# Kernel tuning notes

Hardware: AMD Instinct MI355X
Metric: run time of the kernel (lower is better)

Reference implementation:

```python
import jax, jax.numpy as jnp
import numpy as np

B, N, D = 4, 2048, 512
H, DH = 8, 64  # heads, dim_head; inner_dim = H*DH = 512
SCALE = DH ** -0.5


def setup_inputs() -> dict:
    key = jax.random.key(0)
    kx, kw = jax.random.split(key)
    x = jax.random.normal(kx, (B, N, D), dtype=jnp.float32)
    # torch Linear weight layout: [out_features=3*H*DH, in_features=D]
    W_qkv = jax.random.normal(kw, (3 * H * DH, D), dtype=jnp.float32) * 0.02
    return {"x": x, "W_qkv": W_qkv}


def reference(x, W_qkv):
    b, n, d = x.shape
    # qkv projection (no bias since qkv_bias=False)
    qkv = x @ W_qkv.T                                  # [b, n, 3*H*DH]
    qkv = qkv.reshape(b, n, 3, H, DH).transpose(2, 0, 3, 1, 4)  # [3, b, H, n, DH]
    q, k, v = qkv[0], qkv[1], qkv[2]
    # shifted query: q_cross[t] = q[t-1] for t>=1, q_cross[0] = q[0]
    q_cross = jnp.concatenate([q[:, :, :1, :], q[:, :, :-1, :]], axis=2)
    scores = jnp.einsum("bhqd,bhkd->bhqk", q_cross * SCALE, k)  # [b, H, n, n]
    attn = jax.nn.softmax(scores, axis=-1)
    out = jnp.einsum("bhqk,bhkd->bhqd", attn, v)       # [b, H, n, DH]
    out = out.transpose(0, 2, 1, 3).reshape(b, n, H * DH)
    # to_out is Dropout(0.0) -> identity in eval / p=0
    return out
```

## Files before the change

### kernel.cpp

```cpp
#include <hip/hip_runtime.h>
#include <hip/hip_bf16.h>
#include <stdint.h>

typedef __bf16 bf16_t;
typedef float floatx4 __attribute__((ext_vector_type(4)));
typedef __bf16 bf16x8 __attribute__((ext_vector_type(8)));
typedef __bf16 bf16x4 __attribute__((ext_vector_type(4)));
typedef unsigned int uintx4 __attribute__((ext_vector_type(4)));

#define QSCALE 0.1803368801111204f

__device__ __forceinline__ void gl2lds16(const bf16_t* g, bf16_t* l) {
    __builtin_amdgcn_global_load_lds(
        (const __attribute__((address_space(1))) unsigned int*)g,
        (__attribute__((address_space(3))) unsigned int*)l,
        16, 0, 0);
}

__device__ __forceinline__ unsigned pk2(float lo, float hi) {
    unsigned short a = __builtin_bit_cast(unsigned short, (bf16_t)lo);
    unsigned short b = __builtin_bit_cast(unsigned short, (bf16_t)hi);
    return (unsigned)a | ((unsigned)b << 16);
}

__global__ __launch_bounds__(256) void convert_kernel(const float* __restrict__ x,
                                                      bf16_t* __restrict__ xb,
                                                      const float* __restrict__ w,
                                                      bf16_t* __restrict__ wb,
                                                      int nx4) {
    int i = blockIdx.x * 256 + threadIdx.x;
    const float* in; bf16_t* out; int j;
    if (i < nx4) { in = x; out = xb; j = i; }
    else         { in = w; out = wb; j = i - nx4; }
    float4 v = ((const float4*)in)[j];
    bf16x4 o;
    o.x = (bf16_t)v.x; o.y = (bf16_t)v.y; o.z = (bf16_t)v.z; o.w = (bf16_t)v.w;
    ((bf16x4*)out)[j] = o;
}

__global__ __launch_bounds__(256) void qkv_gemm(const bf16_t* __restrict__ X,
                                                const bf16_t* __restrict__ W,
                                                bf16_t* __restrict__ Q,
                                                bf16_t* __restrict__ K,
                                                bf16_t* __restrict__ Vt)
{
    __shared__ bf16_t As[128 * 64];
    __shared__ bf16_t Bs[128 * 64];

    const int tid  = threadIdx.x;
    const int wave = tid >> 6;
    const int lane = tid & 63;
    const int quad = lane >> 4;
    const int lrow = lane & 15;
    const int t7g  = lrow & 7;
    const int bm0 = blockIdx.x * 128;
    const int bn0 = blockIdx.y * 128;
    const int mw = (wave >> 1) * 64;
    const int nw = (wave & 1) * 64;
    const int wbase = tid & 192;

    floatx4 acc[4][4];
#pragma unroll
    for (int i = 0; i < 4; i++)
#pragma unroll
        for (int j = 0; j < 4; j++) acc[i][j] = (floatx4)0.0f;

#pragma unroll 1
    for (int kb = 0; kb < 8; ++kb) {
        const int k0 = kb * 64;
        __syncthreads();
#pragma unroll
        for (int r = 0; r < 4; ++r) {
            int c = r * 256 + tid;
            int row = c >> 3, kc = c & 7;
            int skc = kc ^ (row & 7);
            gl2lds16(X + (size_t)(bm0 + row) * 512 + k0 + skc * 8,
                     As + (size_t)(r * 256 + wbase) * 8);
        }
#pragma unroll
        for (int r = 0; r < 4; ++r) {
            int c = r * 256 + tid;
            int row = c >> 3, kc = c & 7;
            int skc = kc ^ (row & 7);
            gl2lds16(W + (size_t)(bn0 + row) * 512 + k0 + skc * 8,
                     Bs + (size_t)(r * 256 + wbase) * 8);
        }
        __syncthreads();
#pragma unroll
        for (int ks = 0; ks < 2; ++ks) {
            bf16x8 af[4], bfr[4];
#pragma unroll
            for (int mi = 0; mi < 4; mi++)
                af[mi] = *(const bf16x8*)(As + (mw + mi * 16 + lrow) * 64 + (((ks * 4 + quad) ^ t7g) << 3));
#pragma unroll
            for (int ni = 0; ni < 4; ni++)
                bfr[ni] = *(const bf16x8*)(Bs + (nw + ni * 16 + lrow) * 64 + (((ks * 4 + quad) ^ t7g) << 3));
#pragma unroll
            for (int mi = 0; mi < 4; mi++)
#pragma unroll
                for (int ni = 0; ni < 4; ni++)
                    acc[mi][ni] = __builtin_amdgcn_mfma_f32_16x16x32_bf16(af[mi], bfr[ni], acc[mi][ni], 0, 0, 0);
        }
    }

#pragma unroll
    for (int mi = 0; mi < 4; mi++) {
        int mbase = bm0 + mw + mi * 16 + quad * 4;
        int b = mbase >> 11, n = mbase & 2047;
#pragma unroll
        for (int ni = 0; ni < 4; ni++) {
            int o = bn0 + nw + ni * 16 + lrow;
            int s  = o >> 9;
            int h  = (o >> 6) & 7;
            int dh = o & 63;
            int bh = b * 8 + h;
            if (s == 2) {
                bf16x4 pv;
#pragma unroll
                for (int r = 0; r < 4; r++) pv[r] = (bf16_t)acc[mi][ni][r];
                *(bf16x4*)(Vt + ((size_t)bh * 64 + dh) * 2048 + n) = pv;
            } else if (s == 0) {
#pragma unroll
                for (int r = 0; r < 4; r++)
                    Q[((size_t)bh * 2048 + n + r) * 64 + dh] = (bf16_t)(acc[mi][ni][r] * QSCALE);
            } else {
#pragma unroll
                for (int r = 0; r < 4; r++)
                    K[((size_t)bh * 2048 + n + r) * 64 + dh] = (bf16_t)acc[mi][ni][r];
            }
        }
    }
}

__device__ __forceinline__ void stage_tile(const bf16_t* __restrict__ kb,
                                           const bf16_t* __restrict__ vb,
                                           int kt, bf16_t* ksbuf, bf16_t* vsbuf,
                                           int wave, int lane) {
#pragma unroll
    for (int part = 0; part < 2; ++part) {
        int ch  = part * 256 + wave * 64 + lane;
        int row = ch >> 3, cc = ch & 7;
        int scc = cc ^ (row & 7);
        bf16_t* ldst = ksbuf + (size_t)(part * 256 + wave * 64) * 8;
        gl2lds16(kb + ((size_t)(kt * 64 + row)) * 64 + scc * 8, ldst);
        bf16_t* ldst2 = vsbuf + (size_t)(part * 256 + wave * 64) * 8;
        gl2lds16(vb + (size_t)row * 2048 + kt * 64 + scc * 8, ldst2);
    }
}

__global__ __launch_bounds__(256, 5) void flash_attn(const bf16_t* __restrict__ Q,
                                                     const bf16_t* __restrict__ K,
                                                     const bf16_t* __restrict__ Vt,
                                                     float* __restrict__ Out)
{
    __shared__ bf16_t Ks[2][64 * 64];
    __shared__ bf16_t Vs[2][64 * 64];

    const int tid  = threadIdx.x;
    const int wave = tid >> 6;
    const int lane = tid & 63;
    const int quad = lane >> 4;
    const int c    = lane & 15;
    const int t7   = c & 7;
    const int qhalf = wave >> 1;
    const int khalf = wave & 1;
    const int qt = blockIdx.x;
    const int bh = blockIdx.y;
    const int b = bh >> 3, h = bh & 7;

    const int bw    = ((c & 4) << 1) | ((c & 8) >> 1) | (c & 3);
    const int brow7 = bw & 7;

    bf16x8 qf[2][2];
#pragma unroll
    for (int mt = 0; mt < 2; ++mt) {
        int qg  = qt * 64 + qhalf * 32 + mt * 16 + c;
        int src = (qg == 0) ? 0 : qg - 1;
        const bf16_t* qbase = Q + ((size_t)bh * 2048 + src) * 64;
        qf[mt][0] = *(const bf16x8*)(qbase + quad * 8);
        qf[mt][1] = *(const bf16x8*)(qbase + 32 + quad * 8);
    }

    floatx4 o[2][4];
#pragma unroll
    for (int mt = 0; mt < 2; ++mt)
#pragma unroll
        for (int i = 0; i < 4; i++) o[mt][i] = (floatx4)0.0f;
    float lacc[2] = {0.f, 0.f};

    const bf16_t* kb = K + ((size_t)bh * 2048) * 64;
    const bf16_t* vb = Vt + ((size_t)bh * 64) * 2048;

    stage_tile(kb, vb, 0, Ks[0], Vs[0], wave, lane);

#pragma unroll 1
    for (int kt = 0; kt < 32; ++kt) {
        const int buf = kt & 1;
        __syncthreads();
        if (kt < 31)
            stage_tile(kb, vb, kt + 1, Ks[buf ^ 1], Vs[buf ^ 1], wave, lane);

        const bf16_t* ks = Ks[buf];
        const bf16_t* vs = Vs[buf];

        floatx4 s[2][2];
        __builtin_amdgcn_s_setprio(1);
#pragma unroll
        for (int nt = 0; nt < 2; ++nt) {
            const bf16_t* krow = ks + (khalf * 32 + nt * 16 + bw) * 64;
            bf16x8 kf0 = *(const bf16x8*)(krow + ((quad ^ brow7) << 3));
            bf16x8 kf1 = *(const bf16x8*)(krow + (((4 + quad) ^ brow7) << 3));
#pragma unroll
            for (int mt = 0; mt < 2; ++mt) {
                floatx4 t = (floatx4)0.0f;
                t = __builtin_amdgcn_mfma_f32_16x16x32_bf16(kf0, qf[mt][0], t, 0, 0, 0);
                t = __builtin_amdgcn_mfma_f32_16x16x32_bf16(kf1, qf[mt][1], t, 0, 0, 0);
                s[mt][nt] = t;
            }
        }
        __builtin_amdgcn_s_setprio(0);

        bf16x8 pfrag[2];
#pragma unroll
        for (int mt = 0; mt < 2; ++mt) {
            float pe[2][4];
#pragma unroll
            for (int nt = 0; nt < 2; ++nt)
#pragma unroll
                for (int r = 0; r < 4; ++r) {
                    float p = __builtin_amdgcn_exp2f(s[mt][nt][r]);
                    lacc[mt] += p;
                    pe[nt][r] = p;
                }
            unsigned A0 = pk2(pe[0][0], pe[0][1]);
            unsigned A1 = pk2(pe[0][2], pe[0][3]);
            unsigned B0 = pk2(pe[1][0], pe[1][1]);
            unsigned B1 = pk2(pe[1][2], pe[1][3]);
            auto r0 = __builtin_amdgcn_permlane32_swap((int)A0, (int)B0, false, false);
            auto r1 = __builtin_amdgcn_permlane32_swap((int)A1, (int)B1, false, false);
            uintx4 fd;
            fd.x = (unsigned)r0[0];
            fd.y = (unsigned)r1[0];
            fd.z = (unsigned)r0[1];
            fd.w = (unsigned)r1[1];
            pfrag[mt] = __builtin_bit_cast(bf16x8, fd);
        }

        __builtin_amdgcn_s_setprio(1);
#pragma unroll
        for (int sub = 0; sub < 4; ++sub) {
            const bf16_t* vrow = vs + (sub * 16 + c) * 64;
            bf16x8 vf = *(const bf16x8*)(vrow + (((khalf * 4 + quad) ^ t7) << 3));
            o[0][sub] = __builtin_amdgcn_mfma_f32_16x16x32_bf16(pfrag[0], vf, o[0][sub], 0, 0, 0);
            o[1][sub] = __builtin_amdgcn_mfma_f32_16x16x32_bf16(pfrag[1], vf, o[1][sub], 0, 0, 0);
        }
        __builtin_amdgcn_s_setprio(0);
    }

#pragma unroll
    for (int mt = 0; mt < 2; ++mt) {
        lacc[mt] += __shfl_xor(lacc[mt], 16, 64);
        lacc[mt] += __shfl_xor(lacc[mt], 32, 64);
    }

    __syncthreads();
    float* obuf = (float*)Ks;
    float* lbuf = (float*)Vs;
    if (khalf == 1) {
#pragma unroll
        for (int mt = 0; mt < 2; ++mt)
#pragma unroll
            for (int sub = 0; sub < 4; ++sub)
                *(floatx4*)(obuf + qhalf * 2048 + (mt * 4 + sub) * 256 + lane * 4) = o[mt][sub];
        if (lane < 16) {
#pragma unroll
            for (int mt = 0; mt < 2; ++mt)
                lbuf[qhalf * 32 + mt * 16 + c] = lacc[mt];
        }
    }
    __syncthreads();
    if (khalf == 0) {
#pragma unroll
        for (int mt = 0; mt < 2; ++mt)
#pragma unroll
            for (int sub = 0; sub < 4; ++sub)
                o[mt][sub] += *(const floatx4*)(obuf + qhalf * 2048 + (mt * 4 + sub) * 256 + lane * 4);
#pragma unroll
        for (int mt = 0; mt < 2; ++mt)
            lacc[mt] += lbuf[qhalf * 32 + mt * 16 + c];

        float* ob = Out + (size_t)b * 2048 * 512 + (size_t)h * 64;
#pragma unroll
        for (int mt = 0; mt < 2; ++mt) {
            int n0 = qt * 64 + qhalf * 32 + mt * 16 + quad * 4;
#pragma unroll
            for (int r = 0; r < 4; r++) {
                float lr = __shfl(lacc[mt], quad * 4 + r, 64);
                float inv = 1.0f / lr;
                float* orow = ob + (size_t)(n0 + r) * 512;
#pragma unroll
                for (int sub = 0; sub < 4; ++sub)
                    orow[sub * 16 + c] = o[mt][sub][r] * inv;
            }
        }
    }
}

extern "C" void kernel_launch(void* const* d_in, const int* in_sizes, int n_in,
                              void* d_out, int out_size, void* d_ws, size_t ws_size,
                              hipStream_t stream) {
    const float* x = (const float*)d_in[0];
    const float* w = (const float*)d_in[1];
    float* out = (float*)d_out;

    char* ws = (char*)d_ws;
    bf16_t* xb = (bf16_t*)(ws);
    bf16_t* wb = (bf16_t*)(ws + 8388608);
    bf16_t* q  = (bf16_t*)(ws + 9961472);
    bf16_t* k  = (bf16_t*)(ws + 18350080);
    bf16_t* vt = (bf16_t*)(ws + 26738688);

    convert_kernel<<<4864, 256, 0, stream>>>(x, xb, w, wb, 1048576);
    qkv_gemm<<<dim3(64, 12), 256, 0, stream>>>(xb, wb, q, k, vt);
    flash_attn<<<dim3(32, 32), 256, 0, stream>>>(q, k, vt, out);
}
```

Measured before the change: 144.7 us.

## Double-buffer QKV GEMM, shrink N tile, and add XCD-aware block swizzles

The QKV GEMM now double-buffers LDS tiles so the global-to-LDS loads for the next K block are issued before the current block's MFMAs run, and it drops the second barrier per iteration. The N tile shrinks from 128 to 64, doubling the grid to 1536 blocks and using a 3-blocks-per-SM launch bound. Both the GEMM and flash attention remap block indices so blocks sharing data land on the same XCD for L2 reuse, and s_setprio is raised around the MFMA bursts. In exchange, the GEMM does less reuse per tile and uses more LDS.

After: 140.9 us. -2.6%, faster.

```diff
diff --git a/kernel.cpp b/kernel.cpp
--- a/kernel.cpp
+++ b/kernel.cpp
@@ -38,14 +38,14 @@
     ((bf16x4*)out)[j] = o;
 }
 
-__global__ __launch_bounds__(256) void qkv_gemm(const bf16_t* __restrict__ X,
-                                                const bf16_t* __restrict__ W,
-                                                bf16_t* __restrict__ Q,
-                                                bf16_t* __restrict__ K,
-                                                bf16_t* __restrict__ Vt)
+__global__ __launch_bounds__(256, 3) void qkv_gemm(const bf16_t* __restrict__ X,
+                                                   const bf16_t* __restrict__ W,
+                                                   bf16_t* __restrict__ Q,
+                                                   bf16_t* __restrict__ K,
+                                                   bf16_t* __restrict__ Vt)
 {
-    __shared__ bf16_t As[128 * 64];
-    __shared__ bf16_t Bs[128 * 64];
+    __shared__ bf16_t As[2][128 * 64];
+    __shared__ bf16_t Bs[2][64 * 64];
 
     const int tid  = threadIdx.x;
     const int wave = tid >> 6;
@@ -53,53 +53,78 @@
     const int quad = lane >> 4;
     const int lrow = lane & 15;
     const int t7g  = lrow & 7;
-    const int bm0 = blockIdx.x * 128;
-    const int bn0 = blockIdx.y * 128;
+    const int wbase = tid & 192;
+
+    int raw = blockIdx.x;
+    int xcd = raw & 7;
+    int idx = raw >> 3;
+    int bx  = xcd * 8 + idx / 24;
+    int by  = idx - (idx / 24) * 24;
+    const int bm0 = bx * 128;
+    const int bn0 = by * 64;
     const int mw = (wave >> 1) * 64;
-    const int nw = (wave & 1) * 64;
-    const int wbase = tid & 192;
-
-    floatx4 acc[4][4];
+    const int nw = (wave & 1) * 32;
+
+    floatx4 acc[4][2];
 #pragma unroll
     for (int i = 0; i < 4; i++)
 #pragma unroll
-        for (int j = 0; j < 4; j++) acc[i][j] = (floatx4)0.0f;
+        for (int j = 0; j < 2; j++) acc[i][j] = (floatx4)0.0f;
+
+    const bf16_t* xb  = X + (size_t)bm0 * 512;
+    const bf16_t* wbp = W + (size_t)bn0 * 512;
+    const bf16_t* srcA[4];
+    const bf16_t* srcB[2];
+#pragma unroll
+    for (int r = 0; r < 4; ++r) {
+        int c = r * 256 + tid;
+        int row = c >> 3, kc = c & 7;
+        int skc = kc ^ (row & 7);
+        srcA[r] = xb + (size_t)row * 512 + skc * 8;
+    }
+#pragma unroll
+    for (int r = 0; r < 2; ++r) {
+        int c = r * 256 + tid;
+        int row = c >> 3, kc = c & 7;
+        int skc = kc ^ (row & 7);
+        srcB[r] = wbp + (size_t)row * 512 + skc * 8;
+    }
+
+    auto STAGE = [&](int bufI, int k0) {
+#pragma unroll
+        for (int r = 0; r < 4; ++r)
+            gl2lds16(srcA[r] + k0, As[bufI] + (size_t)(r * 256 + wbase) * 8);
+#pragma unroll
+        for (int r = 0; r < 2; ++r)
+            gl2lds16(srcB[r] + k0, Bs[bufI] + (size_t)(r * 256 + wbase) * 8);
+    };
+
+    STAGE(0, 0);
 
 #pragma unroll 1
     for (int kb = 0; kb < 8; ++kb) {
-        const int k0 = kb * 64;
+        const int buf = kb & 1;
         __syncthreads();
-#pragma unroll
-        for (int r = 0; r < 4; ++r) {
-            int c = r * 256 + tid;
-            int row = c >> 3, kc = c & 7;
-            int skc = kc ^ (row & 7);
-            gl2lds16(X + (size_t)(bm0 + row) * 512 + k0 + skc * 8,
-                     As + (size_t)(r * 256 + wbase) * 8);
-        }
-#pragma unroll
-        for (int r = 0; r < 4; ++r) {
-            int c = r * 256 + tid;
-            int row = c >> 3, kc = c & 7;
-            int skc = kc ^ (row & 7);
-            gl2lds16(W + (size_t)(bn0 + row) * 512 + k0 + skc * 8,
-                     Bs + (size_t)(r * 256 + wbase) * 8);
-        }
-        __syncthreads();
+        if (kb < 7) STAGE(buf ^ 1, (kb + 1) * 64);
+
+        const bf16_t* as = As[buf];
+        const bf16_t* bs = Bs[buf];
 #pragma unroll
         for (int ks = 0; ks < 2; ++ks) {
-            bf16x8 af[4], bfr[4];
+            bf16x8 af[4], bfr[2];
 #pragma unroll
             for (int mi = 0; mi < 4; mi++)
-                af[mi] = *(const bf16x8*)(As + (mw + mi * 16 + lrow) * 64 + (((ks * 4 + quad) ^ t7g) << 3));
-#pragma unroll
-            for (int ni = 0; ni < 4; ni++)
-                bfr[ni] = *(const bf16x8*)(Bs + (nw + ni * 16 + lrow) * 64 + (((ks * 4 + quad) ^ t7g) << 3));
+                af[mi] = *(const bf16x8*)(as + (mw + mi * 16 + lrow) * 64 + (((ks * 4 + quad) ^ t7g) << 3));
+#pragma unroll
+            for (int ni = 0; ni < 2; ni++)
+                bfr[ni] = *(const bf16x8*)(bs + (nw + ni * 16 + lrow) * 64 + (((ks * 4 + quad) ^ t7g) << 3));
+            __builtin_amdgcn_s_setprio(1);
 #pragma unroll
             for (int mi = 0; mi < 4; mi++)
 #pragma unroll
-                for (int ni = 0; ni < 4; ni++)
+                for (int ni = 0; ni < 2; ni++)
                     acc[mi][ni] = __builtin_amdgcn_mfma_f32_16x16x32_bf16(af[mi], bfr[ni], acc[mi][ni], 0, 0, 0);
+            __builtin_amdgcn_s_setprio(0);
         }
     }
 
@@ -108,7 +133,7 @@
         int mbase = bm0 + mw + mi * 16 + quad * 4;
         int b = mbase >> 11, n = mbase & 2047;
 #pragma unroll
-        for (int ni = 0; ni < 4; ni++) {
+        for (int ni = 0; ni < 2; ni++) {
             int o = bn0 + nw + ni * 16 + lrow;
             int s  = o >> 9;
             int h  = (o >> 6) & 7;
@@ -164,8 +189,11 @@
     const int t7   = c & 7;
     const int qhalf = wave >> 1;
     const int khalf = wave & 1;
-    const int qt = blockIdx.x;
-    const int bh = blockIdx.y;
+
+    int raw = blockIdx.x + (blockIdx.y << 5);
+    int swz = (raw & 7) * 128 + (raw >> 3);
+    const int qt = swz & 31;
+    const int bh = swz >> 5;
     const int b = bh >> 3, h = bh & 7;
 
     const int bw    = ((c & 4) << 1) | ((c & 8) >> 1) | (c & 3);
@@ -321,6 +349,6 @@
     bf16_t* vt = (bf16_t*)(ws + 26738688);
 
     convert_kernel<<<4864, 256, 0, stream>>>(x, xb, w, wb, 1048576);
-    qkv_gemm<<<dim3(64, 12), 256, 0, stream>>>(xb, wb, q, k, vt);
+    qkv_gemm<<<1536, 256, 0, stream>>>(xb, wb, q, k, vt);
     flash_attn<<<dim3(32, 32), 256, 0, stream>>>(q, k, vt, out);
 }
```
